# Kernel tuning notes

Hardware: AMD Instinct MI355X
Metric: run time of the kernel (lower is better)

Reference implementation:

```python
import jax, jax.numpy as jnp
import numpy as np

B, T, F, H = 2048, 50, 256, 256
PREVIOUS_VISIT = 50  # number of recurrence steps


def setup_inputs() -> dict:
    key = jax.random.key(0)
    k1, k2, k3, k4 = jax.random.split(key, 4)
    scale = 0.05  # keep gates in a sane range
    return {
        "input_context": jax.random.normal(k1, (B, T, F), dtype=jnp.float32),
        "W": jax.random.normal(k2, (F, 4 * H), dtype=jnp.float32) * scale,
        "U": jax.random.normal(k3, (H, 4 * H), dtype=jnp.float32) * scale,
        "b": jax.random.normal(k4, (4 * H,), dtype=jnp.float32) * scale,
    }


def reference(input_context, W, U, b):
    # Keras LSTMCell math, gate order i, f, g(cell candidate), o.
    batch = input_context.shape[0]
    hidden = U.shape[0]
    h0 = jnp.zeros((batch, hidden), dtype=input_context.dtype)
    c0 = jnp.zeros((batch, hidden), dtype=input_context.dtype)

    def step(carry, x_t):
        h, c = carry
        z = x_t @ W + h @ U + b  # [B, 4H]
        i, f, g, o = jnp.split(z, 4, axis=-1)
        i = jax.nn.sigmoid(i)
        f = jax.nn.sigmoid(f)
        g = jnp.tanh(g)
        o = jax.nn.sigmoid(o)
        c_new = f * c + i * g
        h_new = o * jnp.tanh(c_new)
        return (h_new, c_new), None

    # scan over time: [PV, B, F]
    xs = jnp.swapaxes(input_context[:, :PREVIOUS_VISIT, :], 0, 1)
    (h_fin, c_fin), _ = jax.lax.scan(step, (h0, c0), xs)
    # original returns (output_forward, state_forward=[h, c]); h == output
    return h_fin, c_fin
```

## Files before the change

### kernel.cpp

```cpp
#include <hip/hip_runtime.h>


#define B_ 2048
#define T_ 50
#define F_ 256
#define H_ 256
#define NZ 1024

typedef __attribute__((ext_vector_type(8))) short short8;
typedef __attribute__((ext_vector_type(4))) float f32x4;
typedef __attribute__((ext_vector_type(4))) int i32x4;
typedef unsigned short ushort_t;
typedef unsigned int uint_t;

__device__ __forceinline__ ushort_t f2bf(float f) {
    uint_t u = __float_as_uint(f);
    return (ushort_t)((u + 0x7FFFu + ((u >> 16) & 1u)) >> 16);
}
__device__ __forceinline__ uint_t pack2bf(float lo, float hi) {
    return (uint_t)f2bf(lo) | ((uint_t)f2bf(hi) << 16);
}
__device__ __forceinline__ float bf2f(ushort_t u) {
    return __uint_as_float(((uint_t)u) << 16);
}
__device__ __forceinline__ float sigm(float z) {
    return __builtin_amdgcn_rcpf(1.0f + __builtin_amdgcn_exp2f(z * -1.44269504f));
}
__device__ __forceinline__ float tanh_f(float z) {
    return 2.0f * __builtin_amdgcn_rcpf(1.0f + __builtin_amdgcn_exp2f(z * -2.88539008f)) - 1.0f;
}
__device__ __forceinline__ float xz_at(uint2 u, int j) {
    uint_t v = (j < 2) ? u.x : u.y;
    v = (j & 1) ? (v >> 16) : (v & 0xFFFFu);
    return bf2f((ushort_t)v);
}

__global__ void pack_w(const float* __restrict__ Wm, ushort_t* __restrict__ W2) {
    int gid  = blockIdx.x * 256 + threadIdx.x;
    int lane = gid & 63;
    int nf   = (gid >> 6) & 7;
    int w    = (gid >> 9) & 7;
    int kf   = (gid >> 12) & 7;
    int col = (nf >> 1) * 256 + w * 32 + (nf & 1) * 16 + (lane & 15);
    int kb  = kf * 32 + (lane >> 4) * 8;
    short8 v;
#pragma unroll
    for (int e = 0; e < 8; ++e)
        v[e] = (short)f2bf(Wm[(size_t)(kb + e) * NZ + col]);
    *(short8*)(W2 + ((((size_t)kf * 8 + w) * 8 + nf) * 64 + lane) * 8) = v;
}

__global__ void pack_scale(const float* __restrict__ Um,
                           float* __restrict__ scq, float* __restrict__ scd) {
    int j    = (blockIdx.x * 256 + threadIdx.x) >> 6;
    int lane = threadIdx.x & 63;
    float mx = 0.f;
#pragma unroll
    for (int i = 0; i < H_ / 64; ++i)
        mx = fmaxf(mx, fabsf(Um[(size_t)(i * 64 + lane) * NZ + j]));
#pragma unroll
    for (int off = 32; off; off >>= 1)
        mx = fmaxf(mx, __shfl_down(mx, off));
    if (lane == 0) {
        scq[j] = (mx > 0.f) ? (127.0f / mx) : 0.f;
        scd[j] = mx * (1.0f / 16129.0f);
    }
}

__global__ void pack_u8(const float* __restrict__ Um,
                        const float* __restrict__ scq, char* __restrict__ U8) {
    int gid  = blockIdx.x * 256 + threadIdx.x;
    int lane = gid & 63;
    int nf   = (gid >> 6) & 7;
    int w    = (gid >> 9) & 7;
    int kf   = (gid >> 12) & 3;
    int col = (nf >> 1) * 256 + w * 32 + (nf & 1) * 16 + (lane & 15);
    int k0  = kf * 64 + (lane >> 4) * 16;
    float qs = scq[col];
    union { char c[16]; int4 v; } u;
#pragma unroll
    for (int e = 0; e < 16; ++e)
        u.c[e] = (char)__float2int_rn(Um[(size_t)(k0 + e) * NZ + col] * qs);
    *(int4*)(U8 + (((size_t)(kf * 8 + w) * 8 + nf) << 10) + (size_t)lane * 16) = u.v;
}

__global__ __launch_bounds__(512, 2) void xw_gemm(
    const float* __restrict__ x, const float* __restrict__ bias,
    const ushort_t* __restrict__ W2, ushort_t* __restrict__ xz2) {
    __shared__ __align__(16) ushort_t As[64 * 256];

    const int tid = threadIdx.x;
    const int t = blockIdx.x, rb = blockIdx.y, row0 = rb * 64;
    const int w = tid >> 6, lane = tid & 63, r16 = lane & 15, q = lane >> 4;

    {
        int sr = tid >> 4, sc = tid & 15;
#pragma unroll
        for (int rr = 0; rr < 64; rr += 32) {
            const float* xp = x + ((size_t)(row0 + rr + sr) * T_ + t) * F_ + sc * 16;
            float4 f0 = *(const float4*)(xp + 0);
            float4 f1 = *(const float4*)(xp + 4);
            float4 f2 = *(const float4*)(xp + 8);
            float4 f3 = *(const float4*)(xp + 12);
            uint4 u0 = {pack2bf(f0.x, f0.y), pack2bf(f0.z, f0.w),
                        pack2bf(f1.x, f1.y), pack2bf(f1.z, f1.w)};
            uint4 u1 = {pack2bf(f2.x, f2.y), pack2bf(f2.z, f2.w),
                        pack2bf(f3.x, f3.y), pack2bf(f3.z, f3.w)};
            int c0 = (2 * sc) ^ (sr & 7), c1 = (2 * sc + 1) ^ (sr & 7);
            *(uint4*)&As[(rr + sr) * 256 + c0 * 8] = u0;
            *(uint4*)&As[(rr + sr) * 256 + c1 * 8] = u1;
        }
    }
    float bcol[8];
#pragma unroll
    for (int nf = 0; nf < 8; ++nf)
        bcol[nf] = bias[(nf >> 1) * 256 + w * 32 + (nf & 1) * 16 + r16];
    __syncthreads();

    f32x4 acc[4][8];
#pragma unroll
    for (int m = 0; m < 4; ++m)
#pragma unroll
        for (int nf = 0; nf < 8; ++nf) acc[m][nf] = (f32x4){0.f, 0.f, 0.f, 0.f};
    short8 SB0[8], SB1[8];

#define LOADB(BUF, KF_)                                                       \
    _Pragma("unroll") for (int nf = 0; nf < 8; ++nf)                          \
        BUF[nf] = *(const short8*)(W2 +                                       \
            ((((size_t)(KF_) * 8 + w) * 8 + nf) * 64 + lane) * 8);

#define MF1(BUF, KF_)                                                         \
    do {                                                                      \
        _Pragma("unroll") for (int m = 0; m < 4; ++m) {                       \
            short8 a_ = *(const short8*)&As[(m * 16 + r16) * 256              \
                                            + (((KF_)*4 + q) ^ (r16 & 7)) * 8];\
            _Pragma("unroll") for (int nf = 0; nf < 8; ++nf)                  \
                acc[m][nf] = __builtin_amdgcn_mfma_f32_16x16x32_bf16(         \
                    a_, BUF[nf], acc[m][nf], 0, 0, 0);                        \
        }                                                                     \
    } while (0)

    LOADB(SB0, 0); LOADB(SB1, 1);
    MF1(SB0, 0); LOADB(SB0, 2);
    MF1(SB1, 1); LOADB(SB1, 3);
    MF1(SB0, 2); LOADB(SB0, 4);
    MF1(SB1, 3); LOADB(SB1, 5);
    MF1(SB0, 4); LOADB(SB0, 6);
    MF1(SB1, 5); LOADB(SB1, 7);
    MF1(SB0, 6);
    MF1(SB1, 7);

    uint2* outp = (uint2*)xz2;
#pragma unroll
    for (int m = 0; m < 4; ++m) {
        const size_t cb = (((size_t)t * 64 + (size_t)(rb * 2 + (m >> 1))) * 8 + w) * 16
                        + (size_t)(m & 1) * 8;
#pragma unroll
        for (int nf = 0; nf < 8; ++nf) {
            f32x4 a = acc[m][nf];
            float b = bcol[nf];
            uint2 o = {pack2bf(a[0] + b, a[1] + b), pack2bf(a[2] + b, a[3] + b)};
            outp[(cb + nf) * 64 + lane] = o;
        }
    }
#undef LOADB
#undef MF1
}

__global__ __launch_bounds__(512, 1) void lstm_rec(
    const char* __restrict__ U8, const float* __restrict__ scd,
    const ushort_t* __restrict__ xz2, float* __restrict__ outp, int T) {
    __shared__ __align__(16) char UL[131072];
    __shared__ __align__(16) char hbc[2][4096];

    const int tid = threadIdx.x;
    const int rb = blockIdx.x, row0 = rb * 16;
    const int w = tid >> 6, lane = tid & 63, r16 = lane & 15, q = lane >> 4;

#pragma unroll
    for (int i = 0; i < 16; ++i) {
        int off = i * 8192 + tid * 16;
        __builtin_amdgcn_global_load_lds(
            (const __attribute__((address_space(1))) void*)(U8 + off),
            (__attribute__((address_space(3))) void*)(UL + off),
            16, 0, 0);
    }
    *(uint2*)&hbc[0][tid * 8] = (uint2){0, 0};

    float d[8];
#pragma unroll
    for (int nf = 0; nf < 8; ++nf)
        d[nf] = scd[(nf >> 1) * 256 + w * 32 + (nf & 1) * 16 + r16];

    const uint2* xzp = (const uint2*)xz2;
    const size_t cbconst = (((size_t)(rb >> 1)) * 8 + w) * 16 + (size_t)(rb & 1) * 8;
    const uint2* xzb = xzp + cbconst * 64 + lane;
    const size_t TSTRIDE = (size_t)8192 * 64;

#define AFRAG8(HP_, KF_)                                                      \
    (*(const i32x4*)&(HP_)[r16 * 256 + ((((KF_)*4 + q) ^ (r16 & 7)) << 4)])

    i32x4 acc[8];
    f32x4 creg[2];
    creg[0] = (f32x4){0.f, 0.f, 0.f, 0.f};
    creg[1] = (f32x4){0.f, 0.f, 0.f, 0.f};

    uint2 XZ[8];
#pragma unroll
    for (int k = 0; k < 8; ++k) XZ[k] = xzb[(size_t)k * 64];

    int cur = 0;
    __syncthreads();

#pragma clang loop unroll(disable)
    for (int t = 0; t < T; ++t) {
        const char* hc = hbc[cur];
        char* hn = hbc[cur ^ 1];

        i32x4 S2[8], S3[8];
#pragma unroll
        for (int nf = 0; nf < 8; ++nf)
            S2[nf] = *(const i32x4*)(U8 + (((size_t)(2 * 8 + w) * 8 + nf) << 10)
                                     + (size_t)lane * 16);
#pragma unroll
        for (int nf = 0; nf < 8; ++nf)
            S3[nf] = *(const i32x4*)(U8 + (((size_t)(3 * 8 + w) * 8 + nf) << 10)
                                     + (size_t)lane * 16);
        uint2 XZn[8];
#pragma unroll
        for (int k = 0; k < 8; ++k)
            XZn[k] = xzb[(size_t)(t + 1) * TSTRIDE + (size_t)k * 64];

#pragma unroll
        for (int nf = 0; nf < 8; ++nf) acc[nf] = (i32x4){0, 0, 0, 0};

        __builtin_amdgcn_s_setprio(1);
#pragma unroll
        for (int kf = 0; kf < 2; ++kf) {
            i32x4 a = AFRAG8(hc, kf);
#pragma unroll
            for (int nf = 0; nf < 8; ++nf) {
                i32x4 b = *(const i32x4*)&UL[(((size_t)(kf * 8 + w) * 8 + nf) << 10)
                                             + (size_t)lane * 16];
                acc[nf] = __builtin_amdgcn_mfma_i32_16x16x64_i8(a, b, acc[nf], 0, 0, 0);
            }
        }
        {
            i32x4 a2 = AFRAG8(hc, 2);
#pragma unroll
            for (int nf = 0; nf < 8; ++nf)
                acc[nf] = __builtin_amdgcn_mfma_i32_16x16x64_i8(a2, S2[nf], acc[nf], 0, 0, 0);
            i32x4 a3 = AFRAG8(hc, 3);
#pragma unroll
            for (int nf = 0; nf < 8; ++nf)
                acc[nf] = __builtin_amdgcn_mfma_i32_16x16x64_i8(a3, S3[nf], acc[nf], 0, 0, 0);
        }
        __builtin_amdgcn_s_setprio(0);

#pragma unroll
        for (int hf = 0; hf < 2; ++hf) {
#pragma unroll
            for (int j = 0; j < 4; ++j) {
                float zi = (float)acc[0 + hf][j] * d[0 + hf] + xz_at(XZ[0 + hf], j);
                float zf = (float)acc[2 + hf][j] * d[2 + hf] + xz_at(XZ[2 + hf], j);
                float zg = (float)acc[4 + hf][j] * d[4 + hf] + xz_at(XZ[4 + hf], j);
                float zo = (float)acc[6 + hf][j] * d[6 + hf] + xz_at(XZ[6 + hf], j);
                float ig = sigm(zi);
                float fg = sigm(zf);
                float gg = tanh_f(zg);
                float og = sigm(zo);
                float cn = fg * creg[hf][j] + ig * gg;
                float hv = og * tanh_f(cn);
                creg[hf][j] = cn;
                int row = q * 4 + j;
                int ch  = w * 32 + hf * 16 + r16;
                if (t == T_ - 1) {
                    size_t oi = (size_t)(row0 + row) * H_ + ch;
                    outp[oi] = hv;
                    outp[(size_t)B_ * H_ + oi] = cn;
                } else {
                    hn[row * 256 + (((ch >> 4) ^ (row & 7)) << 4) + (ch & 15)] =
                        (char)__float2int_rn(hv * 127.0f);
                }
            }
        }

#pragma unroll
        for (int k = 0; k < 8; ++k) XZ[k] = XZn[k];

        asm volatile("s_waitcnt lgkmcnt(0)" ::: "memory");
        __builtin_amdgcn_s_barrier();
        cur ^= 1;
    }
#undef AFRAG8
}

extern "C" void kernel_launch(void* const* d_in, const int* in_sizes, int n_in,
                              void* d_out, int out_size, void* d_ws, size_t ws_size,
                              hipStream_t stream) {
    const float* x    = (const float*)d_in[0];
    const float* Wm   = (const float*)d_in[1];
    const float* Um   = (const float*)d_in[2];
    const float* bias = (const float*)d_in[3];

    ushort_t* W2  = (ushort_t*)d_ws;
    char*     U8  = (char*)d_ws + 524288;
    float*    scq = (float*)((char*)d_ws + 786432);
    float*    scd = (float*)((char*)d_ws + 790528);
    ushort_t* xz2 = (ushort_t*)((char*)d_ws + 794624);

    pack_w<<<128, 256, 0, stream>>>(Wm, W2);
    pack_scale<<<256, 256, 0, stream>>>(Um, scq, scd);
    pack_u8<<<64, 256, 0, stream>>>(Um, scq, U8);
    dim3 g1(T_, 32);
    xw_gemm<<<g1, 512, 0, stream>>>(x, bias, W2, xz2);
    lstm_rec<<<128, 512, 0, stream>>>(U8, scd, xz2, (float*)d_out, T_);
}
```

Baseline: 227.4 us.

## Software-pipeline global U and xz loads with inline asm and explicit vmcnt waits

Replaces the per-step compiler-generated global loads of the U slices held outside LDS and of the precomputed input projections with inline-asm loads. They are issued one step ahead and waited on with explicit s_waitcnt vmcnt counters, so memory latency overlaps with the MFMA and gate math of the current step. The final h/c output writes move out of the loop, which removes a per-element branch. The risk is that the hand-counted vmcnt ordering must stay correct. The loop also issues an xz load past the last timestep, which may read beyond the buffer.

```diff
diff --git a/kernel.cpp b/kernel.cpp
--- a/kernel.cpp
+++ b/kernel.cpp
@@ -192,10 +192,52 @@
     for (int nf = 0; nf < 8; ++nf)
         d[nf] = scd[(nf >> 1) * 256 + w * 32 + (nf & 1) * 16 + r16];
 
-    const uint2* xzp = (const uint2*)xz2;
+    const char* baseS2  = U8 + (((size_t)(2 * 8 + w) * 8) << 10) + (size_t)lane * 16;
+    const char* baseS2h = baseS2 + 4096;
+    const char* baseS3  = U8 + (((size_t)(3 * 8 + w) * 8) << 10) + (size_t)lane * 16;
+    const char* baseS3h = baseS3 + 4096;
     const size_t cbconst = (((size_t)(rb >> 1)) * 8 + w) * 16 + (size_t)(rb & 1) * 8;
-    const uint2* xzb = xzp + cbconst * 64 + lane;
-    const size_t TSTRIDE = (size_t)8192 * 64;
+    const char* xzcur = (const char*)((const uint2*)xz2 + cbconst * 64 + lane);
+
+    i32x4 S2[8], S3[8];
+    uint2 XZ[8];
+
+#define ISSUE_S2()                                                            \
+    do {                                                                      \
+        asm volatile("global_load_dwordx4 %0, %1, off"              : "=v"(S2[0]) : "v"(baseS2));  \
+        asm volatile("global_load_dwordx4 %0, %1, off offset:1024"  : "=v"(S2[1]) : "v"(baseS2));  \
+        asm volatile("global_load_dwordx4 %0, %1, off offset:2048"  : "=v"(S2[2]) : "v"(baseS2));  \
+        asm volatile("global_load_dwordx4 %0, %1, off offset:3072"  : "=v"(S2[3]) : "v"(baseS2));  \
+        asm volatile("global_load_dwordx4 %0, %1, off"              : "=v"(S2[4]) : "v"(baseS2h)); \
+        asm volatile("global_load_dwordx4 %0, %1, off offset:1024"  : "=v"(S2[5]) : "v"(baseS2h)); \
+        asm volatile("global_load_dwordx4 %0, %1, off offset:2048"  : "=v"(S2[6]) : "v"(baseS2h)); \
+        asm volatile("global_load_dwordx4 %0, %1, off offset:3072"  : "=v"(S2[7]) : "v"(baseS2h)); \
+    } while (0)
+#define ISSUE_S3()                                                            \
+    do {                                                                      \
+        asm volatile("global_load_dwordx4 %0, %1, off"              : "=v"(S3[0]) : "v"(baseS3));  \
+        asm volatile("global_load_dwordx4 %0, %1, off offset:1024"  : "=v"(S3[1]) : "v"(baseS3));  \
+        asm volatile("global_load_dwordx4 %0, %1, off offset:2048"  : "=v"(S3[2]) : "v"(baseS3));  \
+        asm volatile("global_load_dwordx4 %0, %1, off offset:3072"  : "=v"(S3[3]) : "v"(baseS3));  \
+        asm volatile("global_load_dwordx4 %0, %1, off"              : "=v"(S3[4]) : "v"(baseS3h)); \
+        asm volatile("global_load_dwordx4 %0, %1, off offset:1024"  : "=v"(S3[5]) : "v"(baseS3h)); \
+        asm volatile("global_load_dwordx4 %0, %1, off offset:2048"  : "=v"(S3[6]) : "v"(baseS3h)); \
+        asm volatile("global_load_dwordx4 %0, %1, off offset:3072"  : "=v"(S3[7]) : "v"(baseS3h)); \
+    } while (0)
+#define ISSUE_XZ(P_)                                                          \
+    do {                                                                      \
+        asm volatile("global_load_dwordx2 %0, %1, off"              : "=v"(XZ[0]) : "v"(P_)); \
+        asm volatile("global_load_dwordx2 %0, %1, off offset:512"   : "=v"(XZ[1]) : "v"(P_)); \
+        asm volatile("global_load_dwordx2 %0, %1, off offset:1024"  : "=v"(XZ[2]) : "v"(P_)); \
+        asm volatile("global_load_dwordx2 %0, %1, off offset:1536"  : "=v"(XZ[3]) : "v"(P_)); \
+        asm volatile("global_load_dwordx2 %0, %1, off offset:2048"  : "=v"(XZ[4]) : "v"(P_)); \
+        asm volatile("global_load_dwordx2 %0, %1, off offset:2560"  : "=v"(XZ[5]) : "v"(P_)); \
+        asm volatile("global_load_dwordx2 %0, %1, off offset:3072"  : "=v"(XZ[6]) : "v"(P_)); \
+        asm volatile("global_load_dwordx2 %0, %1, off offset:3584"  : "=v"(XZ[7]) : "v"(P_)); \
+    } while (0)
+#define VMWAIT16()                                                            \
+    do { asm volatile("s_waitcnt vmcnt(16)" ::: "memory");                    \
+         __builtin_amdgcn_sched_barrier(0); } while (0)
 
 #define AFRAG8(HP_, KF_)                                                      \
     (*(const i32x4*)&(HP_)[r16 * 256 + ((((KF_)*4 + q) ^ (r16 & 7)) << 4)])
@@ -204,11 +246,11 @@
     f32x4 creg[2];
     creg[0] = (f32x4){0.f, 0.f, 0.f, 0.f};
     creg[1] = (f32x4){0.f, 0.f, 0.f, 0.f};
-
-    uint2 XZ[8];
-#pragma unroll
-    for (int k = 0; k < 8; ++k) XZ[k] = xzb[(size_t)k * 64];
-
+    f32x4 hreg[2];
+
+    ISSUE_S2();
+    ISSUE_S3();
+    ISSUE_XZ(xzcur);
     int cur = 0;
     __syncthreads();
 
@@ -216,20 +258,6 @@
     for (int t = 0; t < T; ++t) {
         const char* hc = hbc[cur];
         char* hn = hbc[cur ^ 1];
-
-        i32x4 S2[8], S3[8];
-#pragma unroll
-        for (int nf = 0; nf < 8; ++nf)
-            S2[nf] = *(const i32x4*)(U8 + (((size_t)(2 * 8 + w) * 8 + nf) << 10)
-                                     + (size_t)lane * 16);
-#pragma unroll
-        for (int nf = 0; nf < 8; ++nf)
-            S3[nf] = *(const i32x4*)(U8 + (((size_t)(3 * 8 + w) * 8 + nf) << 10)
-                                     + (size_t)lane * 16);
-        uint2 XZn[8];
-#pragma unroll
-        for (int k = 0; k < 8; ++k)
-            XZn[k] = xzb[(size_t)(t + 1) * TSTRIDE + (size_t)k * 64];
 
 #pragma unroll
         for (int nf = 0; nf < 8; ++nf) acc[nf] = (i32x4){0, 0, 0, 0};
@@ -245,18 +273,31 @@
                 acc[nf] = __builtin_amdgcn_mfma_i32_16x16x64_i8(a, b, acc[nf], 0, 0, 0);
             }
         }
+        __builtin_amdgcn_s_setprio(0);
+
+        VMWAIT16();
         {
             i32x4 a2 = AFRAG8(hc, 2);
+            __builtin_amdgcn_s_setprio(1);
 #pragma unroll
             for (int nf = 0; nf < 8; ++nf)
                 acc[nf] = __builtin_amdgcn_mfma_i32_16x16x64_i8(a2, S2[nf], acc[nf], 0, 0, 0);
+            __builtin_amdgcn_s_setprio(0);
+        }
+        ISSUE_S2();
+
+        VMWAIT16();
+        {
             i32x4 a3 = AFRAG8(hc, 3);
+            __builtin_amdgcn_s_setprio(1);
 #pragma unroll
             for (int nf = 0; nf < 8; ++nf)
                 acc[nf] = __builtin_amdgcn_mfma_i32_16x16x64_i8(a3, S3[nf], acc[nf], 0, 0, 0);
-        }
-        __builtin_amdgcn_s_setprio(0);
-
+            __builtin_amdgcn_s_setprio(0);
+        }
+        ISSUE_S3();
+
+        VMWAIT16();
 #pragma unroll
         for (int hf = 0; hf < 2; ++hf) {
 #pragma unroll
@@ -272,26 +313,37 @@
                 float cn = fg * creg[hf][j] + ig * gg;
                 float hv = og * tanh_f(cn);
                 creg[hf][j] = cn;
+                hreg[hf][j] = hv;
                 int row = q * 4 + j;
                 int ch  = w * 32 + hf * 16 + r16;
-                if (t == T_ - 1) {
-                    size_t oi = (size_t)(row0 + row) * H_ + ch;
-                    outp[oi] = hv;
-                    outp[(size_t)B_ * H_ + oi] = cn;
-                } else {
-                    hn[row * 256 + (((ch >> 4) ^ (row & 7)) << 4) + (ch & 15)] =
-                        (char)__float2int_rn(hv * 127.0f);
-                }
+                hn[row * 256 + (((ch >> 4) ^ (row & 7)) << 4) + (ch & 15)] =
+                    (char)__float2int_rn(hv * 127.0f);
             }
         }
 
-#pragma unroll
-        for (int k = 0; k < 8; ++k) XZ[k] = XZn[k];
+        xzcur += (size_t)8192 * 64 * 8;
+        ISSUE_XZ(xzcur);
 
         asm volatile("s_waitcnt lgkmcnt(0)" ::: "memory");
         __builtin_amdgcn_s_barrier();
         cur ^= 1;
     }
+
+#pragma unroll
+    for (int hf = 0; hf < 2; ++hf) {
+#pragma unroll
+        for (int j = 0; j < 4; ++j) {
+            int row = q * 4 + j;
+            int ch  = w * 32 + hf * 16 + r16;
+            size_t oi = (size_t)(row0 + row) * H_ + ch;
+            outp[oi] = hreg[hf][j];
+            outp[(size_t)B_ * H_ + oi] = creg[hf][j];
+        }
+    }
+#undef ISSUE_S2
+#undef ISSUE_S3
+#undef ISSUE_XZ
+#undef VMWAIT16
 #undef AFRAG8
 }
 
```

Result: no change. 230.0 us (+1.2%).
